# Kernel tuning notes

Measured on AMD Instinct MI355X. Metric: run time of the kernel, lower is better.

The kernel has to match this reference:

```python
import jax, jax.numpy as jnp
import numpy as np

NEG_INF = -1e9
START_IDX = 1

def lstm_step(h, c, x_t, Wih, Whh, b):
    g = x_t @ Wih.T + h @ Whh.T + b
    i, f, gg, o = jnp.split(g, 4, axis=-1)  # torch gate order i,f,g,o
    c_new = jax.nn.sigmoid(f) * c + jax.nn.sigmoid(i) * jnp.tanh(gg)
    h_new = jax.nn.sigmoid(o) * jnp.tanh(c_new)
    return h_new, c_new

def masked_lstm(x, valid, Wih, Whh, b):
    # x: [B,S,E], valid: [B,S] bool. Emulates packed-sequence semantics:
    # state frozen and outputs zeroed past each sequence's length.
    B = x.shape[0]; H = Whh.shape[1]
    def step(carry, inp):
        h, c = carry
        x_t, v = inp
        hn, cn = lstm_step(h, c, x_t, Wih, Whh, b)
        v = v[:, None]
        h = jnp.where(v, hn, h); c = jnp.where(v, cn, c)
        return (h, c), jnp.where(v, hn, jnp.zeros_like(hn))
    z = jnp.zeros((B, H), x.dtype)
    (h, c), outs = jax.lax.scan(step, (z, z), (x.transpose(1, 0, 2), valid.T))
    return outs.transpose(1, 0, 2), h, c

def bilstm_encoder(x, lens, Wih_f, Whh_f, b_f, Wih_b, Whh_b, b_b):
    B, S, _ = x.shape
    pos = jnp.arange(S)[None, :]
    valid = pos < lens[:, None]
    out_f, h_f, c_f = masked_lstm(x, valid, Wih_f, Whh_f, b_f)
    # reverse each sequence within its valid length for the backward direction
    rev = jnp.clip(lens[:, None] - 1 - pos, 0, S - 1)  # [B,S]
    x_rev = jnp.take_along_axis(x, rev[:, :, None], axis=1)
    out_r, h_b, c_b = masked_lstm(x_rev, valid, Wih_b, Whh_b, b_b)
    out_b = jnp.take_along_axis(out_r, rev[:, :, None], axis=1) * valid[:, :, None]
    enc = jnp.concatenate([out_f, out_b], -1)          # [B,S,ENC_HID]
    h = jnp.concatenate([h_f, h_b], -1)                # [B,ENC_HID]
    c = jnp.concatenate([c_f, c_b], -1)
    return enc, h, c


def setup_inputs() -> dict:
    key = jax.random.key(0)
    ks = jax.random.split(key, 24)
    B, S, T = 32, 64, 64
    V_SRC, V_TGT, P, E, H2, HD = 50265, 32000, 768, 512, 256, 512
    n = lambda k, sh, s=0.05: (s * jax.random.normal(k, sh)).astype(jnp.float32)
    inp = {
        'xs': jax.random.randint(ks[0], (B, S), 0, V_SRC),
        'x_lens': jax.random.randint(ks[1], (B,), 32, S + 1).astype(jnp.int32),
        'ys': jax.random.randint(ks[2], (B, T + 1), 0, V_TGT),
        'src_emb': n(ks[3], (V_SRC, P)),
        'W_tr': n(ks[4], (E, P)), 'b_tr': jnp.zeros((E,), jnp.float32),
        'Wih_f': n(ks[5], (4 * H2, E)), 'Whh_f': n(ks[6], (4 * H2, H2)), 'b_f': jnp.zeros((4 * H2,), jnp.float32),
        'Wih_b': n(ks[7], (4 * H2, E)), 'Whh_b': n(ks[8], (4 * H2, H2)), 'b_b': jnp.zeros((4 * H2,), jnp.float32),
        'W_attn': n(ks[9], (HD, 2 * HD + HD)), 'b_attn': jnp.zeros((HD,), jnp.float32),
        'v_attn': (jax.random.normal(ks[10], (HD,)) / np.sqrt(HD)).astype(jnp.float32),
        'tgt_emb': n(ks[11], (V_TGT, E)),
        'W_comb': n(ks[12], (HD, E + HD)), 'b_comb': jnp.zeros((HD,), jnp.float32),
        'Wih_d': n(ks[13], (4 * HD, E)), 'Whh_d': n(ks[14], (4 * HD, HD)), 'b_d': jnp.zeros((4 * HD,), jnp.float32),
        'W_out': n(ks[15], (V_TGT, HD)), 'b_out': jnp.zeros((V_TGT,), jnp.float32),
    }
    return inp


def reference(xs, x_lens, ys, src_emb, W_tr, b_tr, Wih_f, Whh_f, b_f,
              Wih_b, Whh_b, b_b, W_attn, b_attn, v_attn, tgt_emb,
              W_comb, b_comb, Wih_d, Whh_d, b_d, W_out, b_out):
    # source embedding (pretrained adapter stub = lookup) + transform
    x = src_emb[xs] @ W_tr.T + b_tr                     # [B,S,E]
    enc, h, c = bilstm_encoder(x, x_lens, Wih_f, Whh_f, b_f, Wih_b, Whh_b, b_b)
    B, S = xs.shape
    T = ys.shape[1] - 1
    HD = Whh_d.shape[1]
    # split attention linear into hidden part and encoder part (precompute latter)
    W_h, W_e = W_attn[:, :2 * HD], W_attn[:, 2 * HD:]
    enc_proj = enc @ W_e.T                              # [B,S,HD]
    src_mask = jnp.arange(S)[None, :] < x_lens[:, None]
    # teacher forcing with ratio 1.0: inputs are [START, ys[:,1:T]]
    tokens = jnp.concatenate([jnp.full((B, 1), START_IDX, ys.dtype), ys[:, 1:T]], axis=1)

    def step(carry, tok):
        h, c = carry
        emb = tgt_emb[tok]                              # [B,E]
        hid = jnp.concatenate([h, c], -1)               # [B,2*HD]
        energy = jnp.tanh(enc_proj + (hid @ W_h.T + b_attn)[:, None, :])
        scores = jnp.where(src_mask, energy @ v_attn, NEG_INF)
        attn = jax.nn.softmax(scores, axis=1)           # [B,S]
        ctx = jnp.einsum('bs,bse->be', attn, enc)
        xi = jax.nn.relu(jnp.concatenate([emb, ctx], -1) @ W_comb.T + b_comb)
        h, c = lstm_step(h, c, xi, Wih_d, Whh_d, b_d)
        out = jax.nn.log_softmax(h @ W_out.T + b_out, axis=-1)
        return (h, c), out

    _, outs = jax.lax.scan(step, (h, c), tokens.T)      # outs: [T,B,V]
    return outs.transpose(1, 0, 2)                      # [B,T,V]
```

## Files before the change

### kernel.cpp

```cpp
#include <hip/hip_runtime.h>
#include <math.h>

#define B_  32
#define S_  64
#define T_  64
#define P_  768
#define E_  512
#define H2_ 256
#define G2_ 1024
#define HD_ 512
#define V_  32000
#define NWG 256

__device__ __forceinline__ float sigf(float x) {
    return 1.0f / (1.0f + __expf(-x));
}
__device__ __forceinline__ float tanh_fast(float x) {
    return 1.0f - 2.0f / (__expf(2.0f * x) + 1.0f);
}

__global__ void k_prep(const int* __restrict__ ys,
                       const float* __restrict__ Whh_f, const float* __restrict__ Whh_b,
                       float* __restrict__ WhhT_f, float* __restrict__ WhhT_b,
                       int* __restrict__ tokens, unsigned* __restrict__ bar)
{
    int i = blockIdx.x * blockDim.x + threadIdx.x;
    int n = gridDim.x * blockDim.x;
    for (int idx = i; idx < G2_ * H2_; idx += n) {
        int k = idx / G2_, g = idx % G2_;
        WhhT_f[idx] = Whh_f[g * H2_ + k];
        WhhT_b[idx] = Whh_b[g * H2_ + k];
    }
    for (int idx = i; idx < T_ * B_; idx += n) {
        int t = idx / B_, b = idx % B_;
        tokens[idx] = (t == 0) ? 1 : ys[b * (T_ + 1) + t];
    }
    for (int idx = i; idx < 160; idx += n) bar[idx] = 0u;
}

__global__ __launch_bounds__(256)
void gemm_f32(const float* __restrict__ A, const int* __restrict__ gidx, int lda,
              const float* __restrict__ W, int ldw, int woff,
              const float* __restrict__ bias,
              float* __restrict__ C, int ldc, int K)
{
    __shared__ __align__(16) float As[16][64];
    __shared__ __align__(16) float Bs[16][64];
    const int m0 = blockIdx.y * 64;
    const int n0 = blockIdx.x * 64;
    const int tid = threadIdx.x;
    const int tm = tid & 15, tn = tid >> 4;
    const int la_m = tid >> 2;
    const int la_k = (tid & 3) * 4;
    float acc[4][4] = {};

    const int am = m0 + la_m;
    const float* arow = A + (long)(gidx ? gidx[am] : am) * lda;
    const float* wrow = W + (long)(n0 + la_m) * ldw + woff;

    for (int k0 = 0; k0 < K; k0 += 16) {
        float4 av = *(const float4*)(arow + k0 + la_k);
        float4 wv = *(const float4*)(wrow + k0 + la_k);
        As[la_k + 0][la_m] = av.x; As[la_k + 1][la_m] = av.y;
        As[la_k + 2][la_m] = av.z; As[la_k + 3][la_m] = av.w;
        Bs[la_k + 0][la_m] = wv.x; Bs[la_k + 1][la_m] = wv.y;
        Bs[la_k + 2][la_m] = wv.z; Bs[la_k + 3][la_m] = wv.w;
        __syncthreads();
        #pragma unroll
        for (int kk = 0; kk < 16; kk++) {
            float4 a = *(const float4*)&As[kk][tm * 4];
            float4 b = *(const float4*)&Bs[kk][tn * 4];
            acc[0][0] += a.x * b.x; acc[0][1] += a.x * b.y; acc[0][2] += a.x * b.z; acc[0][3] += a.x * b.w;
            acc[1][0] += a.y * b.x; acc[1][1] += a.y * b.y; acc[1][2] += a.y * b.z; acc[1][3] += a.y * b.w;
            acc[2][0] += a.z * b.x; acc[2][1] += a.z * b.y; acc[2][2] += a.z * b.z; acc[2][3] += a.z * b.w;
            acc[3][0] += a.w * b.x; acc[3][1] += a.w * b.y; acc[3][2] += a.w * b.z; acc[3][3] += a.w * b.w;
        }
        __syncthreads();
    }
    float b0 = bias ? bias[n0 + tn * 4 + 0] : 0.f;
    float b1 = bias ? bias[n0 + tn * 4 + 1] : 0.f;
    float b2 = bias ? bias[n0 + tn * 4 + 2] : 0.f;
    float b3 = bias ? bias[n0 + tn * 4 + 3] : 0.f;
    #pragma unroll
    for (int i = 0; i < 4; i++) {
        long m = m0 + tm * 4 + i;
        float4 o = make_float4(acc[i][0] + b0, acc[i][1] + b1, acc[i][2] + b2, acc[i][3] + b3);
        *(float4*)&C[m * ldc + n0 + tn * 4] = o;
    }
}

__global__ __launch_bounds__(1024)
void k_encoder(const float* __restrict__ gpre_f, const float* __restrict__ gpre_b,
               const float* __restrict__ WhhT_f, const float* __restrict__ WhhT_b,
               const int* __restrict__ x_lens,
               float* __restrict__ enc, float* __restrict__ hid, float* __restrict__ xh0)
{
    const int b   = blockIdx.x >> 1;
    const int dir = blockIdx.x & 1;
    const float* gpre = dir ? gpre_b : gpre_f;
    const float* WT   = dir ? WhhT_b : WhhT_f;
    const int len = x_lens[b];
    __shared__ float h_lds[H2_];
    __shared__ float g_lds[G2_];
    const int tid = threadIdx.x;
    float c = 0.f;
    if (tid < H2_) h_lds[tid] = 0.f;
    __syncthreads();

    for (int t = 0; t < S_; t++) {
        bool valid = t < len;
        if (valid) {
            int s_in = dir ? (len - 1 - t) : t;
            float acc = gpre[(long)(b * S_ + s_in) * G2_ + tid];
            #pragma unroll 8
            for (int k = 0; k < H2_; k++)
                acc += h_lds[k] * WT[k * G2_ + tid];
            g_lds[tid] = acc;
            __syncthreads();
            if (tid < H2_) {
                float gi = g_lds[tid], gf = g_lds[H2_ + tid];
                float gg = g_lds[2 * H2_ + tid], go = g_lds[3 * H2_ + tid];
                c = sigf(gf) * c + sigf(gi) * tanh_fast(gg);
                float hn = sigf(go) * tanh_fast(c);
                h_lds[tid] = hn;
                enc[(long)(b * S_ + s_in) * E_ + dir * H2_ + tid] = hn;
            }
            __syncthreads();
        } else {
            if (tid < H2_)
                enc[(long)(b * S_ + t) * E_ + dir * H2_ + tid] = 0.f;
        }
    }
    if (tid < H2_) {
        hid[b * 1024 + dir * H2_ + tid]       = h_lds[tid];
        hid[b * 1024 + 512 + dir * H2_ + tid] = c;
        xh0[b * 1024 + 512 + dir * H2_ + tid] = h_lds[tid];
    }
}

__device__ __forceinline__ void grid_bar(unsigned* bar, int w, int tid)
{
    __syncthreads();
    if (tid == 0) {
        __threadfence();
        unsigned a = __hip_atomic_fetch_add(&bar[16 * (w & 7)], 1u,
                        __ATOMIC_RELAXED, __HIP_MEMORY_SCOPE_AGENT);
        unsigned target = (a >> 5) + 1u;
        if ((a & 31u) == 31u) {
            unsigned m = __hip_atomic_fetch_add(&bar[128], 1u,
                            __ATOMIC_RELAXED, __HIP_MEMORY_SCOPE_AGENT);
            if ((m & 7u) == 7u)
                __hip_atomic_store(&bar[144], (m >> 3) + 1u,
                                   __ATOMIC_RELAXED, __HIP_MEMORY_SCOPE_AGENT);
        }
        while (__hip_atomic_load(&bar[144], __ATOMIC_RELAXED,
                                 __HIP_MEMORY_SCOPE_AGENT) < target)
            __builtin_amdgcn_s_sleep(8);
        __threadfence();
    }
    __syncthreads();
}

__global__ __launch_bounds__(256, 1)
void k_decoder(const float* __restrict__ enc, const float* __restrict__ encp,
               const float* __restrict__ embW,
               const float* __restrict__ W_attn, const float* __restrict__ b_attn,
               const float* __restrict__ v_attn, const float* __restrict__ W_comb,
               const float* __restrict__ Wih_d, const float* __restrict__ Whh_d,
               const float* __restrict__ b_d,
               const int* __restrict__ x_lens,
               float* __restrict__ hid, float* __restrict__ xh0,
               float* __restrict__ xh1, float* __restrict__ attq,
               float* __restrict__ ctxg, float* __restrict__ Hall,
               unsigned* __restrict__ bar)
{
    const int w = blockIdx.x;
    const int tid = threadIdx.x;

    __shared__ float WdL[8 * 1028];
    __shared__ float WhL[4 * 1032];
    __shared__ float WcL[4 * 520];
    __shared__ float red[256];
    __shared__ float bsc[832];
    __shared__ float g_l[8 * 33];

    for (int i = tid; i < 8 * 1024; i += 256) {
        int lr = i >> 10, k = i & 1023;
        int row = 512 * (lr & 3) + 2 * w + (lr >> 2);
        WdL[lr * 1028 + k] = (k < 512) ? Wih_d[row * 512 + k]
                                       : Whh_d[row * 512 + (k - 512)];
    }
    for (int i = tid; i < 4 * 1024; i += 256) {
        int lr = i >> 10, k = i & 1023;
        WhL[lr * 1032 + k] = W_attn[(long)(4 * (w >> 1) + lr) * 1536 + k];
    }
    for (int i = tid; i < 4 * 512; i += 256) {
        int lr = i >> 9, k = i & 511;
        WcL[lr * 520 + k] = W_comb[(long)(4 * (w >> 1) + lr) * 1024 + 512 + k];
    }
    __syncthreads();

    const int o  = tid >> 2;
    const int ks = tid & 3;
    const int bl = o >> 2, lr = o & 3;
    const int ab = 16 * (w & 1) + bl;
    const int an = 4 * (w >> 1) + lr;
    const int r8 = tid & 7, b8 = tid >> 3;

    for (int t = 0; t < T_; t++) {
        float* xh_cur  = (t & 1) ? xh1 : xh0;
        float* xh_next = (t & 1) ? xh0 : xh1;

        {
            const float* hr = hid + ab * 1024;
            const float* wr = WhL + lr * 1032;
            float acc = 0.f;
            #pragma unroll 8
            for (int i = 0; i < 64; i++) {
                int k = 16 * i + 4 * ks;
                float4 a = *(const float4*)(hr + k);
                float4 v = *(const float4*)(wr + k);
                acc += a.x * v.x + a.y * v.y + a.z * v.z + a.w * v.w;
            }
            red[tid] = acc;
            __syncthreads();
            if (tid < 64) {
                int b2 = 16 * (w & 1) + (tid >> 2);
                int n2 = 4 * (w >> 1) + (tid & 3);
                float s = red[tid * 4] + red[tid * 4 + 1]
                        + red[tid * 4 + 2] + red[tid * 4 + 3];
                attq[b2 * 512 + n2] = s + b_attn[n2];
            }
        }
        grid_bar(bar, w, tid);

        if (w < 32) {
            float* aq   = bsc;
            float* part = bsc + 512;
            float* p    = bsc + 768;
            aq[tid]       = attq[w * 512 + tid];
            aq[tid + 256] = attq[w * 512 + 256 + tid];
            __syncthreads();
            {
                int s = tid >> 2, q = tid & 3;
                const float* ep = encp + (long)(w * S_ + s) * 512;
                float acc = 0.f;
                #pragma unroll 4
                for (int i = 0; i < 128; i++) {
                    int e = q + 4 * i;
                    acc += v_attn[e] * tanh_fast(ep[e] + aq[e]);
                }
                part[s * 4 + q] = acc;
            }
            __syncthreads();
            if (tid < 64) {
                float sc = part[tid * 4] + part[tid * 4 + 1]
                         + part[tid * 4 + 2] + part[tid * 4 + 3];
                if (tid >= x_lens[w]) sc = -1e9f;
                float m = sc;
                for (int off = 32; off; off >>= 1) m = fmaxf(m, __shfl_xor(m, off));
                float e = __expf(sc - m);
                float sum = e;
                for (int off = 32; off; off >>= 1) sum += __shfl_xor(sum, off);
                p[tid] = e / sum;
            }
            __syncthreads();
            float c0 = 0.f, c1 = 0.f;
            for (int s2 = 0; s2 < S_; s2++) {
                float pp = p[s2];
                const float* er = enc + (long)(w * S_ + s2) * 512;
                c0 += pp * er[tid];
                c1 += pp * er[tid + 256];
            }
            ctxg[w * 512 + tid]       = c0;
            ctxg[w * 512 + 256 + tid] = c1;
        }
        grid_bar(bar, w, tid);

        {
            const float* cr = ctxg + ab * 512;
            const float* wr = WcL + lr * 520;
            float acc = 0.f;
            #pragma unroll 8
            for (int i = 0; i < 32; i++) {
                int k = 16 * i + 4 * ks;
                float4 a = *(const float4*)(cr + k);
                float4 v = *(const float4*)(wr + k);
                acc += a.x * v.x + a.y * v.y + a.z * v.z + a.w * v.w;
            }
            red[tid] = acc;
            __syncthreads();
            if (tid < 64) {
                int b2 = 16 * (w & 1) + (tid >> 2);
                int n2 = 4 * (w >> 1) + (tid & 3);
                float s = red[tid * 4] + red[tid * 4 + 1]
                        + red[tid * 4 + 2] + red[tid * 4 + 3];
                float val = s + embW[((long)t * 32 + b2) * 512 + n2];
                xh_cur[b2 * 1024 + n2] = fmaxf(val, 0.f);
            }
        }
        grid_bar(bar, w, tid);

        {
            const float* ar = xh_cur + b8 * 1024;
            const float* wl = WdL + r8 * 1028;
            float acc = 0.f;
            #pragma unroll 8
            for (int q = 0; q < 256; q++) {
                float4 a = *(const float4*)(ar + 4 * q);
                float4 v = *(const float4*)(wl + 4 * q);
                acc += a.x * v.x + a.y * v.y + a.z * v.z + a.w * v.w;
            }
            int row = 512 * (r8 & 3) + 2 * w + (r8 >> 2);
            g_l[r8 * 33 + b8] = acc + b_d[row];
            __syncthreads();
            if (tid < 64) {
                int bb = tid & 31, hl = tid >> 5;
                int hu = 2 * w + hl;
                float gi = g_l[(hl * 4 + 0) * 33 + bb];
                float gf = g_l[(hl * 4 + 1) * 33 + bb];
                float gg = g_l[(hl * 4 + 2) * 33 + bb];
                float go = g_l[(hl * 4 + 3) * 33 + bb];
                float c_old = hid[bb * 1024 + 512 + hu];
                float c_new = sigf(gf) * c_old + sigf(gi) * tanh_fast(gg);
                float h_new = sigf(go) * tanh_fast(c_new);
                hid[bb * 1024 + hu] = h_new;
                hid[bb * 1024 + 512 + hu] = c_new;
                xh_next[bb * 1024 + 512 + hu] = h_new;
                Hall[((long)bb * T_ + t) * 512 + hu] = h_new;
            }
        }
        grid_bar(bar, w, tid);
    }
}

__global__ __launch_bounds__(256)
void k_lse(const float* __restrict__ Cl, float* __restrict__ lse)
{
    const int r = blockIdx.x;
    const float* row = Cl + (long)r * V_;
    const int tid = threadIdx.x;
    __shared__ float red[4];
    float m = -1e30f;
    for (int i = tid; i < V_; i += 256) m = fmaxf(m, row[i]);
    for (int off = 32; off; off >>= 1) m = fmaxf(m, __shfl_xor(m, off));
    int w = tid >> 6;
    if ((tid & 63) == 0) red[w] = m;
    __syncthreads();
    m = fmaxf(fmaxf(red[0], red[1]), fmaxf(red[2], red[3]));
    __syncthreads();
    float s = 0.f;
    for (int i = tid; i < V_; i += 256) s += __expf(row[i] - m);
    for (int off = 32; off; off >>= 1) s += __shfl_xor(s, off);
    if ((tid & 63) == 0) red[w] = s;
    __syncthreads();
    if (tid == 0) {
        s = red[0] + red[1] + red[2] + red[3];
        lse[r] = m + __logf(s);
    }
}

__global__ void k_logsub(float* __restrict__ C, const float* __restrict__ lse)
{
    long n4 = (long)2048 * V_ / 4;
    long stride = (long)gridDim.x * blockDim.x;
    for (long i = (long)blockIdx.x * blockDim.x + threadIdx.x; i < n4; i += stride) {
        float4 v = ((float4*)C)[i];
        float l = lse[(i * 4) / V_];
        v.x -= l; v.y -= l; v.z -= l; v.w -= l;
        ((float4*)C)[i] = v;
    }
}

extern "C" void kernel_launch(void* const* d_in, const int* in_sizes, int n_in,
                              void* d_out, int out_size, void* d_ws, size_t ws_size,
                              hipStream_t stream)
{
    const int*   xs     = (const int*)  d_in[0];
    const int*   x_lens = (const int*)  d_in[1];
    const int*   ys     = (const int*)  d_in[2];
    const float* src_emb= (const float*)d_in[3];
    const float* W_tr   = (const float*)d_in[4];
    const float* b_tr   = (const float*)d_in[5];
    const float* Wih_f  = (const float*)d_in[6];
    const float* Whh_f  = (const float*)d_in[7];
    const float* b_f    = (const float*)d_in[8];
    const float* Wih_b  = (const float*)d_in[9];
    const float* Whh_b  = (const float*)d_in[10];
    const float* b_b    = (const float*)d_in[11];
    const float* W_attn = (const float*)d_in[12];
    const float* b_attn = (const float*)d_in[13];
    const float* v_attn = (const float*)d_in[14];
    const float* tgt_emb= (const float*)d_in[15];
    const float* W_comb = (const float*)d_in[16];
    const float* b_comb = (const float*)d_in[17];
    const float* Wih_d  = (const float*)d_in[18];
    const float* Whh_d  = (const float*)d_in[19];
    const float* b_d    = (const float*)d_in[20];
    const float* W_out  = (const float*)d_in[21];
    const float* b_out  = (const float*)d_in[22];
    float* out = (float*)d_out;

    float* ws = (float*)d_ws;
    size_t off = 0;
    auto alloc = [&](size_t n) { float* p = ws + off; off += n; return p; };
    float* x      = alloc(2048 * 512);
    float* gpre_f = alloc(2048 * 1024);
    float* gpre_b = alloc(2048 * 1024);
    float* enc    = alloc(2048 * 512);
    float* encp   = alloc(2048 * 512);
    float* embW   = alloc(2048 * 512);
    float* Hall   = alloc(2048 * 512);
    float* hid    = alloc(32 * 1024);
    float* xh0    = alloc(32 * 1024);
    float* xh1    = alloc(32 * 1024);
    float* attq   = alloc(32 * 512);
    float* ctx    = alloc(32 * 512);
    float* WhhTf  = alloc(256 * 1024);
    float* WhhTb  = alloc(256 * 1024);
    float* lse    = alloc(2048);
    int*   tokens = (int*)alloc(2048);
    unsigned* bar = (unsigned*)alloc(160);
    (void)ws_size; (void)n_in; (void)in_sizes; (void)out_size;

    k_prep<<<512, 256, 0, stream>>>(ys, Whh_f, Whh_b, WhhTf, WhhTb, tokens, bar);

    gemm_f32<<<dim3(512 / 64, 2048 / 64), 256, 0, stream>>>(src_emb, xs, P_, W_tr, P_, 0, b_tr, x, 512, P_);
    gemm_f32<<<dim3(1024 / 64, 2048 / 64), 256, 0, stream>>>(x, nullptr, 512, Wih_f, 512, 0, b_f, gpre_f, 1024, 512);
    gemm_f32<<<dim3(1024 / 64, 2048 / 64), 256, 0, stream>>>(x, nullptr, 512, Wih_b, 512, 0, b_b, gpre_b, 1024, 512);

    k_encoder<<<64, 1024, 0, stream>>>(gpre_f, gpre_b, WhhTf, WhhTb, x_lens, enc, hid, xh0);

    gemm_f32<<<dim3(512 / 64, 2048 / 64), 256, 0, stream>>>(enc, nullptr, 512, W_attn, 1536, 1024, nullptr, encp, 512, 512);
    gemm_f32<<<dim3(512 / 64, 2048 / 64), 256, 0, stream>>>(tgt_emb, tokens, 512, W_comb, 1024, 0, b_comb, embW, 512, 512);

    {
        void* args[] = { (void*)&enc, (void*)&encp, (void*)&embW, (void*)&W_attn,
                         (void*)&b_attn, (void*)&v_attn, (void*)&W_comb,
                         (void*)&Wih_d, (void*)&Whh_d, (void*)&b_d, (void*)&x_lens,
                         (void*)&hid, (void*)&xh0, (void*)&xh1, (void*)&attq,
                         (void*)&ctx, (void*)&Hall, (void*)&bar };
        hipLaunchCooperativeKernel((void*)k_decoder, dim3(NWG), dim3(256), args, 0, stream);
    }

    gemm_f32<<<dim3(V_ / 64, 2048 / 64), 256, 0, stream>>>(Hall, nullptr, 512, W_out, 512, 0, b_out, out, V_, 512);
    k_lse<<<2048, 256, 0, stream>>>(out, lse);
    k_logsub<<<8192, 256, 0, stream>>>(out, lse);
}
```

Measured before the change: 8.328 ms.

## Rework decoder grid barrier, split recurrent matvec early, fuse LSE and subtract

Replaces the atomic-counter grid barrier with a two-level flag tree. Each workgroup stores a generation flag, 8 leader groups poll 32 flags each with wavefront-wide loads, and group 0 publishes the release. The h@Whh part of the decoder LSTM gate matvec now runs before the first barrier, so the post-barrier gate step only needs the 512-wide xi input. The attention-query and combine matvecs are repartitioned to 2 rows per workgroup, and the W_comb slice is read from global memory instead of LDS. The log-softmax normalisation becomes a single per-row kernel that computes the LSE and subtracts it, which removes one full pass over the logits and one launch. Risks include the cost of flag polling and the extra global reads of W_comb.

After: 8.286 ms. Within noise of the previous version (-0.5%).

```diff
diff --git a/kernel.cpp b/kernel.cpp
--- a/kernel.cpp
+++ b/kernel.cpp
@@ -35,7 +35,7 @@
         int t = idx / B_, b = idx % B_;
         tokens[idx] = (t == 0) ? 1 : ys[b * (T_ + 1) + t];
     }
-    for (int idx = i; idx < 160; idx += n) bar[idx] = 0u;
+    for (int idx = i; idx < 1024; idx += n) bar[idx] = 0u;
 }
 
 __global__ __launch_bounds__(256)
@@ -93,7 +93,7 @@
 void k_encoder(const float* __restrict__ gpre_f, const float* __restrict__ gpre_b,
                const float* __restrict__ WhhT_f, const float* __restrict__ WhhT_b,
                const int* __restrict__ x_lens,
-               float* __restrict__ enc, float* __restrict__ hid, float* __restrict__ xh0)
+               float* __restrict__ enc, float* __restrict__ hid)
 {
     const int b   = blockIdx.x >> 1;
     const int dir = blockIdx.x & 1;
@@ -134,28 +134,44 @@
     if (tid < H2_) {
         hid[b * 1024 + dir * H2_ + tid]       = h_lds[tid];
         hid[b * 1024 + 512 + dir * H2_ + tid] = c;
-        xh0[b * 1024 + 512 + dir * H2_ + tid] = h_lds[tid];
-    }
-}
-
-__device__ __forceinline__ void grid_bar(unsigned* bar, int w, int tid)
+    }
+}
+
+__device__ __forceinline__ void grid_bar(unsigned* bar, int w, int tid, unsigned gen)
 {
     __syncthreads();
     if (tid == 0) {
         __threadfence();
-        unsigned a = __hip_atomic_fetch_add(&bar[16 * (w & 7)], 1u,
-                        __ATOMIC_RELAXED, __HIP_MEMORY_SCOPE_AGENT);
-        unsigned target = (a >> 5) + 1u;
-        if ((a & 31u) == 31u) {
-            unsigned m = __hip_atomic_fetch_add(&bar[128], 1u,
-                            __ATOMIC_RELAXED, __HIP_MEMORY_SCOPE_AGENT);
-            if ((m & 7u) == 7u)
-                __hip_atomic_store(&bar[144], (m >> 3) + 1u,
-                                   __ATOMIC_RELAXED, __HIP_MEMORY_SCOPE_AGENT);
-        }
-        while (__hip_atomic_load(&bar[144], __ATOMIC_RELAXED,
-                                 __HIP_MEMORY_SCOPE_AGENT) < target)
-            __builtin_amdgcn_s_sleep(8);
+        __hip_atomic_store(&bar[w], gen, __ATOMIC_RELAXED, __HIP_MEMORY_SCOPE_AGENT);
+    }
+    if (w < 8 && tid < 64) {
+        bool mine = tid < 32;
+        for (;;) {
+            unsigned v = mine ? __hip_atomic_load(&bar[32 * w + tid],
+                                 __ATOMIC_RELAXED, __HIP_MEMORY_SCOPE_AGENT) : gen;
+            if (__all(v >= gen)) break;
+            __builtin_amdgcn_s_sleep(1);
+        }
+        if (tid == 0)
+            __hip_atomic_store(&bar[512 + 16 * w], gen,
+                               __ATOMIC_RELAXED, __HIP_MEMORY_SCOPE_AGENT);
+    }
+    if (w == 0 && tid < 64) {
+        bool mine = tid < 8;
+        for (;;) {
+            unsigned v = mine ? __hip_atomic_load(&bar[512 + 16 * tid],
+                                 __ATOMIC_RELAXED, __HIP_MEMORY_SCOPE_AGENT) : gen;
+            if (__all(v >= gen)) break;
+            __builtin_amdgcn_s_sleep(1);
+        }
+        if (tid == 0)
+            __hip_atomic_store(&bar[768], gen,
+                               __ATOMIC_RELAXED, __HIP_MEMORY_SCOPE_AGENT);
+    }
+    if (tid == 0) {
+        while (__hip_atomic_load(&bar[768], __ATOMIC_RELAXED,
+                                 __HIP_MEMORY_SCOPE_AGENT) < gen)
+            __builtin_amdgcn_s_sleep(1);
         __threadfence();
     }
     __syncthreads();
@@ -169,20 +185,19 @@
                const float* __restrict__ Wih_d, const float* __restrict__ Whh_d,
                const float* __restrict__ b_d,
                const int* __restrict__ x_lens,
-               float* __restrict__ hid, float* __restrict__ xh0,
-               float* __restrict__ xh1, float* __restrict__ attq,
-               float* __restrict__ ctxg, float* __restrict__ Hall,
-               unsigned* __restrict__ bar)
+               float* __restrict__ hid, float* __restrict__ xi,
+               float* __restrict__ attq, float* __restrict__ ctxg,
+               float* __restrict__ Hall, unsigned* __restrict__ bar)
 {
     const int w = blockIdx.x;
     const int tid = threadIdx.x;
 
     __shared__ float WdL[8 * 1028];
-    __shared__ float WhL[4 * 1032];
-    __shared__ float WcL[4 * 520];
-    __shared__ float red[256];
-    __shared__ float bsc[832];
+    __shared__ float WhL[2 * 1028];
+    __shared__ __align__(16) float red[256];
+    __shared__ __align__(16) float bsc[832];
     __shared__ float g_l[8 * 33];
+    __shared__ float g_ph[8 * 33];
 
     for (int i = tid; i < 8 * 1024; i += 256) {
         int lr = i >> 10, k = i & 1023;
@@ -190,49 +205,48 @@
         WdL[lr * 1028 + k] = (k < 512) ? Wih_d[row * 512 + k]
                                        : Whh_d[row * 512 + (k - 512)];
     }
-    for (int i = tid; i < 4 * 1024; i += 256) {
+    for (int i = tid; i < 2 * 1024; i += 256) {
         int lr = i >> 10, k = i & 1023;
-        WhL[lr * 1032 + k] = W_attn[(long)(4 * (w >> 1) + lr) * 1536 + k];
-    }
-    for (int i = tid; i < 4 * 512; i += 256) {
-        int lr = i >> 9, k = i & 511;
-        WcL[lr * 520 + k] = W_comb[(long)(4 * (w >> 1) + lr) * 1024 + 512 + k];
-    }
-    __syncthreads();
-
-    const int o  = tid >> 2;
-    const int ks = tid & 3;
-    const int bl = o >> 2, lr = o & 3;
-    const int ab = 16 * (w & 1) + bl;
-    const int an = 4 * (w >> 1) + lr;
+        WhL[lr * 1028 + k] = W_attn[(long)(2 * w + lr) * 1536 + k];
+    }
+    __syncthreads();
+
+    const int bA = tid & 31;
+    const int rA = (tid >> 5) & 1;
+    const int ksA = tid >> 6;
     const int r8 = tid & 7, b8 = tid >> 3;
+    unsigned gen = 1;
 
     for (int t = 0; t < T_; t++) {
-        float* xh_cur  = (t & 1) ? xh1 : xh0;
-        float* xh_next = (t & 1) ? xh0 : xh1;
-
         {
-            const float* hr = hid + ab * 1024;
-            const float* wr = WhL + lr * 1032;
+            const float* hq = hid + (long)bA * 1024 + ksA * 256;
+            const float* wr = WhL + rA * 1028 + ksA * 256;
             float acc = 0.f;
             #pragma unroll 8
             for (int i = 0; i < 64; i++) {
-                int k = 16 * i + 4 * ks;
-                float4 a = *(const float4*)(hr + k);
-                float4 v = *(const float4*)(wr + k);
+                float4 a = *(const float4*)(hq + 4 * i);
+                float4 v = *(const float4*)(wr + 4 * i);
                 acc += a.x * v.x + a.y * v.y + a.z * v.z + a.w * v.w;
             }
             red[tid] = acc;
             __syncthreads();
             if (tid < 64) {
-                int b2 = 16 * (w & 1) + (tid >> 2);
-                int n2 = 4 * (w >> 1) + (tid & 3);
-                float s = red[tid * 4] + red[tid * 4 + 1]
-                        + red[tid * 4 + 2] + red[tid * 4 + 3];
-                attq[b2 * 512 + n2] = s + b_attn[n2];
-            }
-        }
-        grid_bar(bar, w, tid);
+                int b2 = tid & 31, r2 = tid >> 5;
+                float s = red[tid] + red[tid + 64] + red[tid + 128] + red[tid + 192];
+                attq[b2 * 512 + 2 * w + r2] = s + b_attn[2 * w + r2];
+            }
+            const float* hr = hid + (long)b8 * 1024;
+            const float* wl = WdL + r8 * 1028 + 512;
+            float acch = 0.f;
+            #pragma unroll 8
+            for (int q = 0; q < 128; q++) {
+                float4 a = *(const float4*)(hr + 4 * q);
+                float4 v = *(const float4*)(wl + 4 * q);
+                acch += a.x * v.x + a.y * v.y + a.z * v.z + a.w * v.w;
+            }
+            g_ph[r8 * 33 + b8] = acch;
+        }
+        grid_bar(bar, w, tid, gen); gen++;
 
         if (w < 32) {
             float* aq   = bsc;
@@ -275,44 +289,42 @@
             ctxg[w * 512 + tid]       = c0;
             ctxg[w * 512 + 256 + tid] = c1;
         }
-        grid_bar(bar, w, tid);
+        grid_bar(bar, w, tid, gen); gen++;
 
         {
-            const float* cr = ctxg + ab * 512;
-            const float* wr = WcL + lr * 520;
+            const float* cr = ctxg + (long)bA * 512 + ksA * 128;
+            const float* wr = W_comb + (long)(2 * w + rA) * 1024 + 512 + ksA * 128;
             float acc = 0.f;
             #pragma unroll 8
             for (int i = 0; i < 32; i++) {
-                int k = 16 * i + 4 * ks;
-                float4 a = *(const float4*)(cr + k);
-                float4 v = *(const float4*)(wr + k);
+                float4 a = *(const float4*)(cr + 4 * i);
+                float4 v = *(const float4*)(wr + 4 * i);
                 acc += a.x * v.x + a.y * v.y + a.z * v.z + a.w * v.w;
             }
             red[tid] = acc;
             __syncthreads();
             if (tid < 64) {
-                int b2 = 16 * (w & 1) + (tid >> 2);
-                int n2 = 4 * (w >> 1) + (tid & 3);
-                float s = red[tid * 4] + red[tid * 4 + 1]
-                        + red[tid * 4 + 2] + red[tid * 4 + 3];
+                int b2 = tid & 31, r2 = tid >> 5;
+                int n2 = 2 * w + r2;
+                float s = red[tid] + red[tid + 64] + red[tid + 128] + red[tid + 192];
                 float val = s + embW[((long)t * 32 + b2) * 512 + n2];
-                xh_cur[b2 * 1024 + n2] = fmaxf(val, 0.f);
-            }
-        }
-        grid_bar(bar, w, tid);
+                xi[b2 * 512 + n2] = fmaxf(val, 0.f);
+            }
+        }
+        grid_bar(bar, w, tid, gen); gen++;
 
         {
-            const float* ar = xh_cur + b8 * 1024;
+            const float* ar = xi + (long)b8 * 512;
             const float* wl = WdL + r8 * 1028;
             float acc = 0.f;
             #pragma unroll 8
-            for (int q = 0; q < 256; q++) {
+            for (int q = 0; q < 128; q++) {
                 float4 a = *(const float4*)(ar + 4 * q);
                 float4 v = *(const float4*)(wl + 4 * q);
                 acc += a.x * v.x + a.y * v.y + a.z * v.z + a.w * v.w;
             }
             int row = 512 * (r8 & 3) + 2 * w + (r8 >> 2);
-            g_l[r8 * 33 + b8] = acc + b_d[row];
+            g_l[r8 * 33 + b8] = acc + g_ph[r8 * 33 + b8] + b_d[row];
             __syncthreads();
             if (tid < 64) {
                 int bb = tid & 31, hl = tid >> 5;
@@ -326,19 +338,18 @@
                 float h_new = sigf(go) * tanh_fast(c_new);
                 hid[bb * 1024 + hu] = h_new;
                 hid[bb * 1024 + 512 + hu] = c_new;
-                xh_next[bb * 1024 + 512 + hu] = h_new;
                 Hall[((long)bb * T_ + t) * 512 + hu] = h_new;
             }
         }
-        grid_bar(bar, w, tid);
+        grid_bar(bar, w, tid, gen); gen++;
     }
 }
 
 __global__ __launch_bounds__(256)
-void k_lse(const float* __restrict__ Cl, float* __restrict__ lse)
+void k_lsesub(float* __restrict__ Cl)
 {
     const int r = blockIdx.x;
-    const float* row = Cl + (long)r * V_;
+    float* row = Cl + (long)r * V_;
     const int tid = threadIdx.x;
     __shared__ float red[4];
     float m = -1e30f;
@@ -354,21 +365,13 @@
     for (int off = 32; off; off >>= 1) s += __shfl_xor(s, off);
     if ((tid & 63) == 0) red[w] = s;
     __syncthreads();
-    if (tid == 0) {
-        s = red[0] + red[1] + red[2] + red[3];
-        lse[r] = m + __logf(s);
-    }
-}
-
-__global__ void k_logsub(float* __restrict__ C, const float* __restrict__ lse)
-{
-    long n4 = (long)2048 * V_ / 4;
-    long stride = (long)gridDim.x * blockDim.x;
-    for (long i = (long)blockIdx.x * blockDim.x + threadIdx.x; i < n4; i += stride) {
-        float4 v = ((float4*)C)[i];
-        float l = lse[(i * 4) / V_];
+    s = red[0] + red[1] + red[2] + red[3];
+    float l = m + __logf(s);
+    float4* r4 = (float4*)row;
+    for (int i = tid; i < V_ / 4; i += 256) {
+        float4 v = r4[i];
         v.x -= l; v.y -= l; v.z -= l; v.w -= l;
-        ((float4*)C)[i] = v;
+        r4[i] = v;
     }
 }
 
@@ -412,15 +415,13 @@
     float* embW   = alloc(2048 * 512);
     float* Hall   = alloc(2048 * 512);
     float* hid    = alloc(32 * 1024);
-    float* xh0    = alloc(32 * 1024);
-    float* xh1    = alloc(32 * 1024);
+    float* xi     = alloc(32 * 512);
     float* attq   = alloc(32 * 512);
-    float* ctx    = alloc(32 * 512);
+    float* ctxg   = alloc(32 * 512);
     float* WhhTf  = alloc(256 * 1024);
     float* WhhTb  = alloc(256 * 1024);
-    float* lse    = alloc(2048);
     int*   tokens = (int*)alloc(2048);
-    unsigned* bar = (unsigned*)alloc(160);
+    unsigned* bar = (unsigned*)alloc(1024);
     (void)ws_size; (void)n_in; (void)in_sizes; (void)out_size;
 
     k_prep<<<512, 256, 0, stream>>>(ys, Whh_f, Whh_b, WhhTf, WhhTb, tokens, bar);
@@ -429,7 +430,7 @@
     gemm_f32<<<dim3(1024 / 64, 2048 / 64), 256, 0, stream>>>(x, nullptr, 512, Wih_f, 512, 0, b_f, gpre_f, 1024, 512);
     gemm_f32<<<dim3(1024 / 64, 2048 / 64), 256, 0, stream>>>(x, nullptr, 512, Wih_b, 512, 0, b_b, gpre_b, 1024, 512);
 
-    k_encoder<<<64, 1024, 0, stream>>>(gpre_f, gpre_b, WhhTf, WhhTb, x_lens, enc, hid, xh0);
+    k_encoder<<<64, 1024, 0, stream>>>(gpre_f, gpre_b, WhhTf, WhhTb, x_lens, enc, hid);
 
     gemm_f32<<<dim3(512 / 64, 2048 / 64), 256, 0, stream>>>(enc, nullptr, 512, W_attn, 1536, 1024, nullptr, encp, 512, 512);
     gemm_f32<<<dim3(512 / 64, 2048 / 64), 256, 0, stream>>>(tgt_emb, tokens, 512, W_comb, 1024, 0, b_comb, embW, 512, 512);
@@ -438,12 +439,11 @@
         void* args[] = { (void*)&enc, (void*)&encp, (void*)&embW, (void*)&W_attn,
                          (void*)&b_attn, (void*)&v_attn, (void*)&W_comb,
                          (void*)&Wih_d, (void*)&Whh_d, (void*)&b_d, (void*)&x_lens,
-                         (void*)&hid, (void*)&xh0, (void*)&xh1, (void*)&attq,
-                         (void*)&ctx, (void*)&Hall, (void*)&bar };
+                         (void*)&hid, (void*)&xi, (void*)&attq, (void*)&ctxg,
+                         (void*)&Hall, (void*)&bar };
         hipLaunchCooperativeKernel((void*)k_decoder, dim3(NWG), dim3(256), args, 0, stream);
     }
 
     gemm_f32<<<dim3(V_ / 64, 2048 / 64), 256, 0, stream>>>(Hall, nullptr, 512, W_out, 512, 0, b_out, out, V_, 512);
-    k_lse<<<2048, 256, 0, stream>>>(out, lse);
-    k_logsub<<<8192, 256, 0, stream>>>(out, lse);
-}
+    k_lsesub<<<2048, 256, 0, stream>>>(out);
+}
```
